# Kernel tuning notes

Measured on AMD Instinct MI355X. Metric: run time of the kernel, lower is better.

## Reference

```python
import jax, jax.numpy as jnp
import numpy as np

E, H, HD = 2048, 32, 64
SCALE = HD ** -0.5


def setup_inputs() -> dict:
    key = jax.random.key(0)
    ks = jax.random.split(key, 11)
    B, T, P = 16, 4, 4096
    S = P + T
    return {
        "hidden_states": jax.random.normal(ks[0], (B, T, E), jnp.float32),
        "past_key": jax.random.normal(ks[1], (1, H, P, HD), jnp.float32),
        "past_value": jax.random.normal(ks[2], (1, H, P, HD), jnp.float32),
        "attention_mask": jnp.zeros((B, 1, T, S), jnp.float32),
        "Wq": jax.random.normal(ks[3], (E, E), jnp.float32) * 0.02,
        "bq": jax.random.normal(ks[4], (E,), jnp.float32) * 0.02,
        "Wk": jax.random.normal(ks[5], (E, E), jnp.float32) * 0.02,
        "bk": jax.random.normal(ks[6], (E,), jnp.float32) * 0.02,
        "Wv": jax.random.normal(ks[7], (E, E), jnp.float32) * 0.02,
        "bv": jax.random.normal(ks[8], (E,), jnp.float32) * 0.02,
        "Wo": jax.random.normal(ks[9], (E, E), jnp.float32) * 0.02,
        "bo": jax.random.normal(ks[10], (E,), jnp.float32) * 0.02,
    }


def _shape(x, B, S):
    # [B,S,E] -> [B,H,S,hd]
    return x.reshape(B, S, H, HD).transpose(0, 2, 1, 3)


def reference(hidden_states, past_key, past_value, attention_mask,
              Wq, bq, Wk, bk, Wv, bv, Wo, bo):
    B, T, _ = hidden_states.shape
    # projections (torch Linear: x @ W.T + b); query pre-scaled
    q = _shape(hidden_states @ Wq.T + bq, B, T) * SCALE   # [B,H,T,hd]
    k_new = _shape(hidden_states @ Wk.T + bk, B, T)       # [B,H,T,hd]
    v_new = _shape(hidden_states @ Wv.T + bv, B, T)
    # cache stored with batch 1, broadcast (torch repeat) to B, then concat
    k_past = jnp.broadcast_to(past_key, (B,) + past_key.shape[1:])
    v_past = jnp.broadcast_to(past_value, (B,) + past_value.shape[1:])
    k = jnp.concatenate([k_past, k_new], axis=2)          # [B,H,S,hd]
    v = jnp.concatenate([v_past, v_new], axis=2)
    scores = jnp.einsum('bhtd,bhsd->bhts', q, k)          # [B,H,T,S]
    scores = scores + attention_mask                      # mask is [B,1,T,S]
    scores = jnp.maximum(scores, jnp.finfo(scores.dtype).min)
    w = jax.nn.softmax(scores, axis=-1)
    out = jnp.einsum('bhts,bhsd->bhtd', w, v)             # [B,H,T,hd]
    out = out.transpose(0, 2, 1, 3).reshape(B, T, E)
    return out @ Wo.T + bo
```

## Files before the change

kernel.cpp:

```cpp
#include <hip/hip_runtime.h>
#include <hip/hip_bf16.h>


typedef float f4 __attribute__((ext_vector_type(4)));
typedef short s8v __attribute__((ext_vector_type(8)));

#define NEG_HUGE (-3.402823466e38f)

__device__ inline unsigned short f2bs(float x) {
  union { float f; unsigned int u; } a; a.f = x;
  unsigned int u = a.u;
  u += 0x7fffu + ((u >> 16) & 1u);
  return (unsigned short)(u >> 16);
}
__device__ inline float bs2f(unsigned short s) {
  union { unsigned int u; float f; } a; a.u = ((unsigned int)s) << 16;
  return a.f;
}
__device__ inline unsigned int pk2(float a, float b) {
  union { __hip_bfloat162 v; unsigned int u; } c;
  c.v = __float22bfloat162_rn(make_float2(a, b));
  return c.u;
}
__device__ inline unsigned long long pack4(float a, float b, float c, float d) {
  return (unsigned long long)pk2(a, b) | ((unsigned long long)pk2(c, d) << 32);
}
__device__ inline s8v cvt8(f4 a, f4 b) {
  union { s8v s; unsigned int u[4]; } r;
  r.u[0] = pk2(a[0], a[1]); r.u[1] = pk2(a[2], a[3]);
  r.u[2] = pk2(b[0], b[1]); r.u[3] = pk2(b[2], b[3]);
  return r.s;
}
__device__ inline f4 mfma16(s8v a, s8v b, f4 c) {
  return __builtin_amdgcn_mfma_f32_16x16x32_bf16(a, b, c, 0, 0, 0);
}
__device__ inline f4 fzero() { f4 z = {0.f,0.f,0.f,0.f}; return z; }
__device__ inline float wave_sum(float v) {
  #pragma unroll
  for (int off = 32; off; off >>= 1) v += __shfl_xor(v, off, 64);
  return v;
}

__global__ __launch_bounds__(256) void k_qkv(
    const float* __restrict__ hs, const float* __restrict__ Wq,
    const float* __restrict__ Wk, const float* __restrict__ Wv,
    float* __restrict__ part) {
  __shared__ __align__(16) unsigned short As[64 * 264];
  const int n0 = blockIdx.x * 64;
  const int ksb = blockIdx.y;
  const int p = n0 >> 11;
  const int c0 = n0 & 2047;
  const float* W = (p == 0) ? Wq : (p == 1) ? Wk : Wv;
  const int t = threadIdx.x, lane = t & 63, w = t >> 6;
  const int cl = lane & 15, quad = lane >> 4;

  f4 acc[4];
  #pragma unroll
  for (int i = 0; i < 4; ++i) acc[i] = fzero();

  const int cw = c0 + w * 16 + cl;
  for (int kt = 0; kt < 2; ++kt) {
    const int k0 = ksb * 512 + kt * 256;
    __syncthreads();
    #pragma unroll
    for (int i = 0; i < 16; ++i) {
      int idx4 = t + (i << 8);
      int row = idx4 >> 6;
      int col = (idx4 & 63) << 2;
      f4 v = *reinterpret_cast<const f4*>(hs + row * 2048 + k0 + col);
      *reinterpret_cast<unsigned long long*>(&As[row * 264 + col]) =
          pack4(v[0], v[1], v[2], v[3]);
    }
    __syncthreads();
    const float* wbase = W + (size_t)cw * 2048 + k0;
    #pragma unroll
    for (int ks2 = 0; ks2 < 8; ++ks2) {
      const int kb = ks2 * 32 + quad * 8;
      f4 w0 = *reinterpret_cast<const f4*>(wbase + kb);
      f4 w1 = *reinterpret_cast<const f4*>(wbase + kb + 4);
      s8v bf = cvt8(w0, w1);
      #pragma unroll
      for (int mt = 0; mt < 4; ++mt) {
        s8v af = *reinterpret_cast<const s8v*>(&As[(mt * 16 + cl) * 264 + kb]);
        acc[mt] = mfma16(af, bf, acc[mt]);
      }
    }
  }
  float* outp = part + (size_t)ksb * 64 * 6144;
  #pragma unroll
  for (int mt = 0; mt < 4; ++mt)
    #pragma unroll
    for (int rg = 0; rg < 4; ++rg) {
      int r = mt * 16 + quad * 4 + rg;
      outp[r * 6144 + n0 + w * 16 + cl] = acc[mt][rg];
    }
}

__global__ __launch_bounds__(256) void k_qkv_red(
    const float* __restrict__ part, const float* __restrict__ bq,
    const float* __restrict__ bk, const float* __restrict__ bv,
    unsigned short* __restrict__ qws, float* __restrict__ knew,
    float* __restrict__ vnew) {
  int idx = blockIdx.x * 256 + threadIdx.x;
  int r = idx / 6144;
  int n = idx - r * 6144;
  float s = part[idx] + part[idx + 393216] + part[idx + 786432] + part[idx + 1179648];
  int c = n & 2047, p = n >> 11;
  int h = c >> 6, d = c & 63;
  int b = r >> 2, tt = r & 3;
  if (p == 0) {
    s = (s + bq[c]) * 0.125f;
    qws[h * 4608 + r * 72 + d] = f2bs(s);
  } else if (p == 1) {
    knew[((h * 16 + b) * 4 + tt) * 64 + d] = s + bk[c];
  } else {
    vnew[((h * 16 + b) * 4 + tt) * 64 + d] = s + bv[c];
  }
}

__global__ __launch_bounds__(256) void k_flash(
    const unsigned short* __restrict__ qws, const float* __restrict__ Kp,
    const float* __restrict__ Vp, const float* __restrict__ mask,
    float* __restrict__ Opart, float* __restrict__ mpart,
    float* __restrict__ lpart) {
  __shared__ __align__(16) unsigned short Pl[64 * 264];
  __shared__ float redm[4 * 64];
  __shared__ float reds[4 * 64];
  const int bx = blockIdx.x;
  const int h = bx & 31, cch = bx >> 5;
  const int s0 = cch * 256;
  const int t = threadIdx.x, lane = t & 63, w = t >> 6;
  const int cl = lane & 15, quad = lane >> 4;
  const float* Kh = Kp + (size_t)h * 4096 * 64;
  const float* Vh = Vp + (size_t)h * 4096 * 64;

  s8v qf[4][2];
  #pragma unroll
  for (int qt = 0; qt < 4; ++qt)
    #pragma unroll
    for (int k2 = 0; k2 < 2; ++k2)
      qf[qt][k2] = *reinterpret_cast<const s8v*>(
          qws + h * 4608 + (qt * 16 + cl) * 72 + k2 * 32 + quad * 8);

  f4 acc[4][4];
  #pragma unroll
  for (int si = 0; si < 4; ++si)
    #pragma unroll
    for (int qt = 0; qt < 4; ++qt) acc[si][qt] = fzero();

  #pragma unroll
  for (int si = 0; si < 4; ++si) {
    const float* kr = Kh + (size_t)(s0 + w * 64 + si * 16 + cl) * 64 + quad * 8;
    #pragma unroll
    for (int k2 = 0; k2 < 2; ++k2) {
      f4 k0v = *reinterpret_cast<const f4*>(kr + k2 * 32);
      f4 k1v = *reinterpret_cast<const f4*>(kr + k2 * 32 + 4);
      s8v ak = cvt8(k0v, k1v);
      #pragma unroll
      for (int qt = 0; qt < 4; ++qt)
        acc[si][qt] = mfma16(ak, qf[qt][k2], acc[si][qt]);
    }
  }

  #pragma unroll
  for (int si = 0; si < 4; ++si)
    #pragma unroll
    for (int qt = 0; qt < 4; ++qt) {
      f4 mv = *reinterpret_cast<const f4*>(
          mask + (size_t)(qt * 16 + cl) * 4100 + s0 + w * 64 + si * 16 + quad * 4);
      #pragma unroll
      for (int rg = 0; rg < 4; ++rg)
        acc[si][qt][rg] = fmaxf(acc[si][qt][rg] + mv[rg], NEG_HUGE);
    }

  #pragma unroll
  for (int qt = 0; qt < 4; ++qt) {
    float m = NEG_HUGE;
    #pragma unroll
    for (int si = 0; si < 4; ++si)
      #pragma unroll
      for (int rg = 0; rg < 4; ++rg) m = fmaxf(m, acc[si][qt][rg]);
    m = fmaxf(m, __shfl_xor(m, 16, 64));
    m = fmaxf(m, __shfl_xor(m, 32, 64));
    if (quad == 0) redm[w * 64 + qt * 16 + cl] = m;
  }
  __syncthreads();

  float mq[4];
  #pragma unroll
  for (int qt = 0; qt < 4; ++qt) {
    int q = qt * 16 + cl;
    mq[qt] = fmaxf(fmaxf(redm[q], redm[64 + q]),
                   fmaxf(redm[128 + q], redm[192 + q]));
    if (w == 0 && quad == 0) mpart[(h * 16 + cch) * 64 + q] = mq[qt];
  }
  #pragma unroll
  for (int qt = 0; qt < 4; ++qt) {
    float sum = 0.f;
    #pragma unroll
    for (int si = 0; si < 4; ++si) {
      f4 e;
      #pragma unroll
      for (int rg = 0; rg < 4; ++rg) {
        e[rg] = __expf(acc[si][qt][rg] - mq[qt]);
        sum += e[rg];
      }
      uint2 pw;
      pw.x = pk2(e[0], e[1]);
      pw.y = pk2(e[2], e[3]);
      *reinterpret_cast<uint2*>(
          &Pl[(qt * 16 + cl) * 264 + w * 64 + si * 16 + quad * 4]) = pw;
    }
    sum += __shfl_xor(sum, 16, 64);
    sum += __shfl_xor(sum, 32, 64);
    if (quad == 0) reds[w * 64 + qt * 16 + cl] = sum;
  }
  __syncthreads();

  if (w == 0 && quad == 0) {
    #pragma unroll
    for (int qt = 0; qt < 4; ++qt) {
      int q = qt * 16 + cl;
      lpart[(h * 16 + cch) * 64 + q] =
          reds[q] + reds[64 + q] + reds[128 + q] + reds[192 + q];
    }
  }

  f4 oacc[4];
  #pragma unroll
  for (int mt = 0; mt < 4; ++mt) oacc[mt] = fzero();
  const int dcol = w * 16 + cl;
  #pragma unroll
  for (int k2 = 0; k2 < 8; ++k2) {
    const int sb = k2 * 32 + quad * 8;
    const float* vb = Vh + (size_t)(s0 + sb) * 64 + dcol;
    f4 v0, v1;
    v0[0] = vb[0];   v0[1] = vb[64];  v0[2] = vb[128]; v0[3] = vb[192];
    v1[0] = vb[256]; v1[1] = vb[320]; v1[2] = vb[384]; v1[3] = vb[448];
    s8v bv = cvt8(v0, v1);
    #pragma unroll
    for (int mt = 0; mt < 4; ++mt) {
      s8v pa = *reinterpret_cast<const s8v*>(&Pl[(mt * 16 + cl) * 264 + sb]);
      oacc[mt] = mfma16(pa, bv, oacc[mt]);
    }
  }
  float* ob = Opart + (size_t)(h * 16 + cch) * 64 * 64;
  #pragma unroll
  for (int mt = 0; mt < 4; ++mt)
    #pragma unroll
    for (int rg = 0; rg < 4; ++rg)
      ob[(mt * 16 + quad * 4 + rg) * 64 + dcol] = oacc[mt][rg];
}

__global__ __launch_bounds__(64) void k_merge(
    const unsigned short* __restrict__ qws, const float* __restrict__ knew,
    const float* __restrict__ vnew, const float* __restrict__ mask,
    const float* __restrict__ Opart, const float* __restrict__ mpart,
    const float* __restrict__ lpart, unsigned short* __restrict__ attn) {
  const int bx = blockIdx.x;
  const int h = bx & 31, b = bx >> 5;
  const int d = threadIdx.x;
  for (int tt = 0; tt < 4; ++tt) {
    const int r = b * 4 + tt;
    float qd = bs2f(qws[h * 4608 + r * 72 + d]);
    float scn[4];
    #pragma unroll
    for (int tp = 0; tp < 4; ++tp) {
      float kn = knew[((h * 16 + b) * 4 + tp) * 64 + d];
      float s = wave_sum(qd * kn);
      s += mask[(size_t)r * 4100 + 4096 + tp];
      scn[tp] = fmaxf(s, NEG_HUGE);
    }
    float mi[16], li[16];
    float mtot = NEG_HUGE;
    #pragma unroll
    for (int i = 0; i < 16; ++i) {
      mi[i] = mpart[(h * 16 + i) * 64 + r];
      li[i] = lpart[(h * 16 + i) * 64 + r];
      mtot = fmaxf(mtot, mi[i]);
    }
    #pragma unroll
    for (int tp = 0; tp < 4; ++tp) mtot = fmaxf(mtot, scn[tp]);
    float ltot = 0.f, od = 0.f;
    #pragma unroll
    for (int i = 0; i < 16; ++i) {
      float fct = __expf(mi[i] - mtot);
      ltot += li[i] * fct;
      od += Opart[((size_t)(h * 16 + i) * 64 + r) * 64 + d] * fct;
    }
    #pragma unroll
    for (int tp = 0; tp < 4; ++tp) {
      float e = __expf(scn[tp] - mtot);
      ltot += e;
      od += e * vnew[((h * 16 + b) * 4 + tp) * 64 + d];
    }
    attn[(size_t)r * 2048 + h * 64 + d] = f2bs(od / ltot);
  }
}

__global__ __launch_bounds__(256) void k_out(
    const unsigned short* __restrict__ attn, const float* __restrict__ Wo,
    float* __restrict__ part) {
  __shared__ __align__(16) unsigned short As[64 * 264];
  const int n0 = blockIdx.x * 64;
  const int ksb = blockIdx.y;
  const int k0 = ksb * 256;
  const int t = threadIdx.x, lane = t & 63, w = t >> 6;
  const int cl = lane & 15, quad = lane >> 4;
  #pragma unroll
  for (int i = 0; i < 8; ++i) {
    int idx8 = t + (i << 8);
    int row = idx8 >> 5;
    int col = (idx8 & 31) << 3;
    *reinterpret_cast<uint4*>(&As[row * 264 + col]) =
        *reinterpret_cast<const uint4*>(attn + (size_t)row * 2048 + k0 + col);
  }
  __syncthreads();
  f4 acc[4];
  #pragma unroll
  for (int i = 0; i < 4; ++i) acc[i] = fzero();
  const int cw = n0 + w * 16 + cl;
  const float* wbase = Wo + (size_t)cw * 2048 + k0;
  #pragma unroll
  for (int ks2 = 0; ks2 < 8; ++ks2) {
    const int kb = ks2 * 32 + quad * 8;
    f4 w0 = *reinterpret_cast<const f4*>(wbase + kb);
    f4 w1 = *reinterpret_cast<const f4*>(wbase + kb + 4);
    s8v bf = cvt8(w0, w1);
    #pragma unroll
    for (int mt = 0; mt < 4; ++mt) {
      s8v af = *reinterpret_cast<const s8v*>(&As[(mt * 16 + cl) * 264 + kb]);
      acc[mt] = mfma16(af, bf, acc[mt]);
    }
  }
  float* op = part + (size_t)ksb * 64 * 2048;
  #pragma unroll
  for (int mt = 0; mt < 4; ++mt)
    #pragma unroll
    for (int rg = 0; rg < 4; ++rg) {
      int r = mt * 16 + quad * 4 + rg;
      op[r * 2048 + n0 + w * 16 + cl] = acc[mt][rg];
    }
}

__global__ __launch_bounds__(256) void k_out_red(
    const float* __restrict__ part, const float* __restrict__ bo,
    float* __restrict__ out) {
  int idx = blockIdx.x * 256 + threadIdx.x;
  int n = idx & 2047;
  float s = bo[n];
  #pragma unroll
  for (int ks = 0; ks < 8; ++ks) s += part[idx + ks * 131072];
  out[idx] = s;
}

extern "C" void kernel_launch(void* const* d_in, const int* in_sizes, int n_in,
                              void* d_out, int out_size, void* d_ws, size_t ws_size,
                              hipStream_t stream) {
  const float* hs   = (const float*)d_in[0];
  const float* pk   = (const float*)d_in[1];
  const float* pv   = (const float*)d_in[2];
  const float* mask = (const float*)d_in[3];
  const float* Wq   = (const float*)d_in[4];
  const float* bq   = (const float*)d_in[5];
  const float* Wk   = (const float*)d_in[6];
  const float* bk   = (const float*)d_in[7];
  const float* Wv   = (const float*)d_in[8];
  const float* bv   = (const float*)d_in[9];
  const float* Wo   = (const float*)d_in[10];
  const float* bo   = (const float*)d_in[11];

  float* f = (float*)d_ws;
  float* qkv_part = f;
  float* o_part   = qkv_part + 1572864;
  float* Opart    = o_part   + 1048576;
  float* mpart    = Opart    + 2097152;
  float* lpart    = mpart    + 32768;
  float* knew     = lpart    + 32768;
  float* vnew     = knew     + 131072;
  unsigned short* qws  = (unsigned short*)(vnew + 131072);
  unsigned short* attn = qws + 147456;

  k_qkv<<<dim3(96, 4), 256, 0, stream>>>(hs, Wq, Wk, Wv, qkv_part);
  k_qkv_red<<<1536, 256, 0, stream>>>(qkv_part, bq, bk, bv, qws, knew, vnew);
  k_flash<<<512, 256, 0, stream>>>(qws, pk, pv, mask, Opart, mpart, lpart);
  k_merge<<<512, 64, 0, stream>>>(qws, knew, vnew, mask, Opart, mpart, lpart, attn);
  k_out<<<dim3(32, 8), 256, 0, stream>>>(attn, Wo, o_part);
  k_out_red<<<512, 256, 0, stream>>>(o_part, bo, (float*)d_out);
}
```

Measured before the change: 210.3 us.

## Raise split-K in QKV GEMM, vectorize reductions, parallelize merge over query rows

The QKV projection now splits K into 8 chunks of 256 instead of 4 chunks of 512, which doubles the grid to 768 blocks and drops the inner K loop and its extra barriers. Both split-K reduction kernels now handle four elements per thread with vector loads, adds and stores. The merge kernel runs one wave per query row (256 threads per block) instead of looping over four rows in a single wave. The cost is twice the partial-sum traffic for QKV and a larger workspace, in exchange for more parallelism in the weight-streaming GEMM.

```diff
diff --git a/kernel.cpp b/kernel.cpp
--- a/kernel.cpp
+++ b/kernel.cpp
@@ -47,46 +47,43 @@
     float* __restrict__ part) {
   __shared__ __align__(16) unsigned short As[64 * 264];
   const int n0 = blockIdx.x * 64;
-  const int ksb = blockIdx.y;
+  const int k0 = blockIdx.y * 256;
   const int p = n0 >> 11;
   const int c0 = n0 & 2047;
   const float* W = (p == 0) ? Wq : (p == 1) ? Wk : Wv;
   const int t = threadIdx.x, lane = t & 63, w = t >> 6;
   const int cl = lane & 15, quad = lane >> 4;
 
+  #pragma unroll
+  for (int i = 0; i < 16; ++i) {
+    int idx4 = t + (i << 8);
+    int row = idx4 >> 6;
+    int col = (idx4 & 63) << 2;
+    f4 v = *reinterpret_cast<const f4*>(hs + row * 2048 + k0 + col);
+    *reinterpret_cast<unsigned long long*>(&As[row * 264 + col]) =
+        pack4(v[0], v[1], v[2], v[3]);
+  }
+  __syncthreads();
+
   f4 acc[4];
   #pragma unroll
   for (int i = 0; i < 4; ++i) acc[i] = fzero();
 
   const int cw = c0 + w * 16 + cl;
-  for (int kt = 0; kt < 2; ++kt) {
-    const int k0 = ksb * 512 + kt * 256;
-    __syncthreads();
-    #pragma unroll
-    for (int i = 0; i < 16; ++i) {
-      int idx4 = t + (i << 8);
-      int row = idx4 >> 6;
-      int col = (idx4 & 63) << 2;
-      f4 v = *reinterpret_cast<const f4*>(hs + row * 2048 + k0 + col);
-      *reinterpret_cast<unsigned long long*>(&As[row * 264 + col]) =
-          pack4(v[0], v[1], v[2], v[3]);
-    }
-    __syncthreads();
-    const float* wbase = W + (size_t)cw * 2048 + k0;
-    #pragma unroll
-    for (int ks2 = 0; ks2 < 8; ++ks2) {
-      const int kb = ks2 * 32 + quad * 8;
-      f4 w0 = *reinterpret_cast<const f4*>(wbase + kb);
-      f4 w1 = *reinterpret_cast<const f4*>(wbase + kb + 4);
-      s8v bf = cvt8(w0, w1);
-      #pragma unroll
-      for (int mt = 0; mt < 4; ++mt) {
-        s8v af = *reinterpret_cast<const s8v*>(&As[(mt * 16 + cl) * 264 + kb]);
-        acc[mt] = mfma16(af, bf, acc[mt]);
-      }
-    }
-  }
-  float* outp = part + (size_t)ksb * 64 * 6144;
+  const float* wbase = W + (size_t)cw * 2048 + k0;
+  #pragma unroll
+  for (int ks2 = 0; ks2 < 8; ++ks2) {
+    const int kb = ks2 * 32 + quad * 8;
+    f4 w0 = *reinterpret_cast<const f4*>(wbase + kb);
+    f4 w1 = *reinterpret_cast<const f4*>(wbase + kb + 4);
+    s8v bf = cvt8(w0, w1);
+    #pragma unroll
+    for (int mt = 0; mt < 4; ++mt) {
+      s8v af = *reinterpret_cast<const s8v*>(&As[(mt * 16 + cl) * 264 + kb]);
+      acc[mt] = mfma16(af, bf, acc[mt]);
+    }
+  }
+  float* outp = part + (size_t)blockIdx.y * 64 * 6144;
   #pragma unroll
   for (int mt = 0; mt < 4; ++mt)
     #pragma unroll
@@ -101,20 +98,38 @@
     const float* __restrict__ bk, const float* __restrict__ bv,
     unsigned short* __restrict__ qws, float* __restrict__ knew,
     float* __restrict__ vnew) {
-  int idx = blockIdx.x * 256 + threadIdx.x;
-  int r = idx / 6144;
-  int n = idx - r * 6144;
-  float s = part[idx] + part[idx + 393216] + part[idx + 786432] + part[idx + 1179648];
-  int c = n & 2047, p = n >> 11;
-  int h = c >> 6, d = c & 63;
-  int b = r >> 2, tt = r & 3;
+  const int i4 = blockIdx.x * 256 + threadIdx.x;
+  const int base = i4 * 4;
+  const int r = base / 6144;
+  const int n = base - r * 6144;
+  f4 s = *reinterpret_cast<const f4*>(part + base);
+  #pragma unroll
+  for (int ks = 1; ks < 8; ++ks) {
+    f4 p2 = *reinterpret_cast<const f4*>(part + (size_t)ks * 393216 + base);
+    #pragma unroll
+    for (int j = 0; j < 4; ++j) s[j] += p2[j];
+  }
+  const int p = n >> 11, c = n & 2047;
+  const int h = c >> 6, d = c & 63;
+  const int b = r >> 2, tt = r & 3;
   if (p == 0) {
-    s = (s + bq[c]) * 0.125f;
-    qws[h * 4608 + r * 72 + d] = f2bs(s);
+    f4 bb = *reinterpret_cast<const f4*>(bq + c);
+    uint2 pw;
+    pw.x = pk2((s[0] + bb[0]) * 0.125f, (s[1] + bb[1]) * 0.125f);
+    pw.y = pk2((s[2] + bb[2]) * 0.125f, (s[3] + bb[3]) * 0.125f);
+    *reinterpret_cast<uint2*>(qws + h * 4608 + r * 72 + d) = pw;
   } else if (p == 1) {
-    knew[((h * 16 + b) * 4 + tt) * 64 + d] = s + bk[c];
+    f4 bb = *reinterpret_cast<const f4*>(bk + c);
+    f4 o;
+    #pragma unroll
+    for (int j = 0; j < 4; ++j) o[j] = s[j] + bb[j];
+    *reinterpret_cast<f4*>(knew + ((h * 16 + b) * 4 + tt) * 64 + d) = o;
   } else {
-    vnew[((h * 16 + b) * 4 + tt) * 64 + d] = s + bv[c];
+    f4 bb = *reinterpret_cast<const f4*>(bv + c);
+    f4 o;
+    #pragma unroll
+    for (int j = 0; j < 4; ++j) o[j] = s[j] + bb[j];
+    *reinterpret_cast<f4*>(vnew + ((h * 16 + b) * 4 + tt) * 64 + d) = o;
   }
 }
 
@@ -237,11 +252,11 @@
     f4 v0, v1;
     v0[0] = vb[0];   v0[1] = vb[64];  v0[2] = vb[128]; v0[3] = vb[192];
     v1[0] = vb[256]; v1[1] = vb[320]; v1[2] = vb[384]; v1[3] = vb[448];
-    s8v bv = cvt8(v0, v1);
+    s8v bvv = cvt8(v0, v1);
     #pragma unroll
     for (int mt = 0; mt < 4; ++mt) {
       s8v pa = *reinterpret_cast<const s8v*>(&Pl[(mt * 16 + cl) * 264 + sb]);
-      oacc[mt] = mfma16(pa, bv, oacc[mt]);
+      oacc[mt] = mfma16(pa, bvv, oacc[mt]);
     }
   }
   float* ob = Opart + (size_t)(h * 16 + cch) * 64 * 64;
@@ -252,50 +267,49 @@
       ob[(mt * 16 + quad * 4 + rg) * 64 + dcol] = oacc[mt][rg];
 }
 
-__global__ __launch_bounds__(64) void k_merge(
+__global__ __launch_bounds__(256) void k_merge(
     const unsigned short* __restrict__ qws, const float* __restrict__ knew,
     const float* __restrict__ vnew, const float* __restrict__ mask,
     const float* __restrict__ Opart, const float* __restrict__ mpart,
     const float* __restrict__ lpart, unsigned short* __restrict__ attn) {
   const int bx = blockIdx.x;
   const int h = bx & 31, b = bx >> 5;
-  const int d = threadIdx.x;
-  for (int tt = 0; tt < 4; ++tt) {
-    const int r = b * 4 + tt;
-    float qd = bs2f(qws[h * 4608 + r * 72 + d]);
-    float scn[4];
-    #pragma unroll
-    for (int tp = 0; tp < 4; ++tp) {
-      float kn = knew[((h * 16 + b) * 4 + tp) * 64 + d];
-      float s = wave_sum(qd * kn);
-      s += mask[(size_t)r * 4100 + 4096 + tp];
-      scn[tp] = fmaxf(s, NEG_HUGE);
-    }
-    float mi[16], li[16];
-    float mtot = NEG_HUGE;
-    #pragma unroll
-    for (int i = 0; i < 16; ++i) {
-      mi[i] = mpart[(h * 16 + i) * 64 + r];
-      li[i] = lpart[(h * 16 + i) * 64 + r];
-      mtot = fmaxf(mtot, mi[i]);
-    }
-    #pragma unroll
-    for (int tp = 0; tp < 4; ++tp) mtot = fmaxf(mtot, scn[tp]);
-    float ltot = 0.f, od = 0.f;
-    #pragma unroll
-    for (int i = 0; i < 16; ++i) {
-      float fct = __expf(mi[i] - mtot);
-      ltot += li[i] * fct;
-      od += Opart[((size_t)(h * 16 + i) * 64 + r) * 64 + d] * fct;
-    }
-    #pragma unroll
-    for (int tp = 0; tp < 4; ++tp) {
-      float e = __expf(scn[tp] - mtot);
-      ltot += e;
-      od += e * vnew[((h * 16 + b) * 4 + tp) * 64 + d];
-    }
-    attn[(size_t)r * 2048 + h * 64 + d] = f2bs(od / ltot);
-  }
+  const int tt = threadIdx.x >> 6;
+  const int d = threadIdx.x & 63;
+  const int r = b * 4 + tt;
+  float qd = bs2f(qws[h * 4608 + r * 72 + d]);
+  float scn[4];
+  #pragma unroll
+  for (int tp = 0; tp < 4; ++tp) {
+    float kn = knew[((h * 16 + b) * 4 + tp) * 64 + d];
+    float s = wave_sum(qd * kn);
+    s += mask[(size_t)r * 4100 + 4096 + tp];
+    scn[tp] = fmaxf(s, NEG_HUGE);
+  }
+  float mi[16], li[16];
+  float mtot = NEG_HUGE;
+  #pragma unroll
+  for (int i = 0; i < 16; ++i) {
+    mi[i] = mpart[(h * 16 + i) * 64 + r];
+    li[i] = lpart[(h * 16 + i) * 64 + r];
+    mtot = fmaxf(mtot, mi[i]);
+  }
+  #pragma unroll
+  for (int tp = 0; tp < 4; ++tp) mtot = fmaxf(mtot, scn[tp]);
+  float ltot = 0.f, od = 0.f;
+  #pragma unroll
+  for (int i = 0; i < 16; ++i) {
+    float fct = __expf(mi[i] - mtot);
+    ltot += li[i] * fct;
+    od += Opart[((size_t)(h * 16 + i) * 64 + r) * 64 + d] * fct;
+  }
+  #pragma unroll
+  for (int tp = 0; tp < 4; ++tp) {
+    float e = __expf(scn[tp] - mtot);
+    ltot += e;
+    od += e * vnew[((h * 16 + b) * 4 + tp) * 64 + d];
+  }
+  attn[(size_t)r * 2048 + h * 64 + d] = f2bs(od / ltot);
 }
 
 __global__ __launch_bounds__(256) void k_out(
@@ -333,7 +347,7 @@
       acc[mt] = mfma16(af, bf, acc[mt]);
     }
   }
-  float* op = part + (size_t)ksb * 64 * 2048;
+  float* op = part + (size_t)ksb * 131072;
   #pragma unroll
   for (int mt = 0; mt < 4; ++mt)
     #pragma unroll
@@ -346,12 +360,19 @@
 __global__ __launch_bounds__(256) void k_out_red(
     const float* __restrict__ part, const float* __restrict__ bo,
     float* __restrict__ out) {
-  int idx = blockIdx.x * 256 + threadIdx.x;
-  int n = idx & 2047;
-  float s = bo[n];
-  #pragma unroll
-  for (int ks = 0; ks < 8; ++ks) s += part[idx + ks * 131072];
-  out[idx] = s;
+  const int i4 = blockIdx.x * 256 + threadIdx.x;
+  f4 s = *reinterpret_cast<const f4*>(part + (size_t)i4 * 4);
+  #pragma unroll
+  for (int ks = 1; ks < 8; ++ks) {
+    f4 p2 = *reinterpret_cast<const f4*>(part + (size_t)ks * 131072 + (size_t)i4 * 4);
+    #pragma unroll
+    for (int j = 0; j < 4; ++j) s[j] += p2[j];
+  }
+  f4 bias = *reinterpret_cast<const f4*>(bo + (i4 & 511) * 4);
+  f4 o;
+  #pragma unroll
+  for (int j = 0; j < 4; ++j) o[j] = s[j] + bias[j];
+  *reinterpret_cast<f4*>(out + (size_t)i4 * 4) = o;
 }
 
 extern "C" void kernel_launch(void* const* d_in, const int* in_sizes, int n_in,
@@ -372,7 +393,7 @@
 
   float* f = (float*)d_ws;
   float* qkv_part = f;
-  float* o_part   = qkv_part + 1572864;
+  float* o_part   = qkv_part + 3145728;
   float* Opart    = o_part   + 1048576;
   float* mpart    = Opart    + 2097152;
   float* lpart    = mpart    + 32768;
@@ -381,10 +402,10 @@
   unsigned short* qws  = (unsigned short*)(vnew + 131072);
   unsigned short* attn = qws + 147456;
 
-  k_qkv<<<dim3(96, 4), 256, 0, stream>>>(hs, Wq, Wk, Wv, qkv_part);
-  k_qkv_red<<<1536, 256, 0, stream>>>(qkv_part, bq, bk, bv, qws, knew, vnew);
+  k_qkv<<<dim3(96, 8), 256, 0, stream>>>(hs, Wq, Wk, Wv, qkv_part);
+  k_qkv_red<<<384, 256, 0, stream>>>(qkv_part, bq, bk, bv, qws, knew, vnew);
   k_flash<<<512, 256, 0, stream>>>(qws, pk, pv, mask, Opart, mpart, lpart);
-  k_merge<<<512, 64, 0, stream>>>(qws, knew, vnew, mask, Opart, mpart, lpart, attn);
+  k_merge<<<512, 256, 0, stream>>>(qws, knew, vnew, mask, Opart, mpart, lpart, attn);
   k_out<<<dim3(32, 8), 256, 0, stream>>>(attn, Wo, o_part);
-  k_out_red<<<512, 256, 0, stream>>>(o_part, bo, (float*)d_out);
-}
+  k_out_red<<<128, 256, 0, stream>>>(o_part, bo, (float*)d_out);
+}
```

Result: faster. 196.6 us (-6.5%).
